# Kernel optimization log

Hardware: AMD Instinct MI355X
Metric: run time of the kernel (lower is better)

Reference implementation:

```python
import jax, jax.numpy as jnp
import numpy as np

HQ, HK, DH = 32, 8, 64
ROPE_BASE = 10000.0


def _rope_tables(T, dtype):
    pos = jnp.arange(T, dtype=jnp.float32)
    inv_freq = 1.0 / (ROPE_BASE ** (jnp.arange(0, DH, 2, dtype=jnp.float32) / DH))
    freqs = pos[:, None] * inv_freq[None, :]          # (T, DH/2)
    cos = jnp.concatenate([jnp.cos(freqs), jnp.cos(freqs)], -1).astype(dtype)  # (T, DH)
    sin = jnp.concatenate([jnp.sin(freqs), jnp.sin(freqs)], -1).astype(dtype)
    return cos, sin


def _rotate_half(t):
    return jnp.concatenate([-t[..., DH // 2:], t[..., :DH // 2]], -1)


def setup_inputs() -> dict:
    key = jax.random.key(0)
    k1, k2, k3, k4 = jax.random.split(key, 4)
    B, T, D = 2, 2048, 2048
    std = 0.02 / np.sqrt(24)
    kv_std = std / np.sqrt(HQ / HK)
    return {
        "x": jax.random.normal(k1, (B, T, D), jnp.float32),
        "Wq": jax.random.normal(k2, (D, HQ * DH), jnp.float32) * std,
        "Wkv": jax.random.normal(k3, (D, 2 * HK * DH), jnp.float32) * kv_std,
        "Wo": jax.random.normal(k4, (HQ * DH, D), jnp.float32) * std,
    }


def reference(x, Wq, Wkv, Wo):
    B, T, D = x.shape
    g = HQ // HK
    scale = DH ** -0.5
    # projections
    q = (x @ Wq).reshape(B, T, HQ, DH).transpose(0, 2, 1, 3)       # (B,Hq,T,Dh)
    kv = (x @ Wkv).reshape(B, T, 2, HK, DH)
    k = kv[:, :, 0].transpose(0, 2, 1, 3)                           # (B,Hk,T,Dh)
    v = kv[:, :, 1].transpose(0, 2, 1, 3)
    # GQA expand: each kv head repeated g times consecutively
    k = jnp.repeat(k, g, axis=1)                                    # (B,Hq,T,Dh)
    v = jnp.repeat(v, g, axis=1)
    # RoPE on q and repeated k
    cos, sin = _rope_tables(T, x.dtype)
    q = q * cos + _rotate_half(q) * sin
    k = k * cos + _rotate_half(k) * sin
    # attention
    scores = jnp.einsum('bhqd,bhkd->bhqk', q, k) * scale            # (B,Hq,T,T)
    causal = jnp.triu(jnp.ones((T, T), bool), 1)
    scores = jnp.where(causal, -jnp.inf, scores)
    attn = jax.nn.softmax(scores.astype(jnp.float32), axis=-1).astype(x.dtype)
    out = jnp.einsum('bhqk,bhkd->bhqd', attn, v)                    # (B,Hq,T,Dh)
    out = out.transpose(0, 2, 1, 3).reshape(B, T, HQ * DH)
    return out @ Wo
```

## Files before the change

kernel.cpp:

```cpp
#include <hip/hip_runtime.h>
#include <hip/hip_bf16.h>

#define DEVI __device__ __forceinline__

typedef __attribute__((ext_vector_type(4))) float f32x4;
typedef __attribute__((ext_vector_type(16))) float f32x16;
typedef __attribute__((ext_vector_type(8))) short s16x8;
typedef __attribute__((ext_vector_type(4))) short s16x4;
typedef __attribute__((ext_vector_type(2))) unsigned u32x2;

DEVI ushort f2bf(float f) {
  union { float f; unsigned u; } v; v.f = f;
  unsigned r = v.u + 0x7FFFu + ((v.u >> 16) & 1u);
  return (ushort)(r >> 16);
}

DEVI void gload_lds16(const void* g, void* l) {
  __builtin_amdgcn_global_load_lds((const __attribute__((address_space(1))) void*)g,
                                   (__attribute__((address_space(3))) void*)l, 16, 0, 0);
}

#define MFMA16 __builtin_amdgcn_mfma_f32_16x16x32_bf16
#define SBAR() __builtin_amdgcn_s_barrier()
#define LGKM0() asm volatile("s_waitcnt lgkmcnt(0)")

DEVI float plswap_max(float x) {
  union { float f; unsigned u; } a; a.f = x;
  u32x2 r = __builtin_amdgcn_permlane32_swap(a.u, a.u, false, false);
  union { unsigned u; float f; } o0, o1; o0.u = r[0]; o1.u = r[1];
  return fmaxf(o0.f, o1.f);
}
DEVI float plswap_sum(float x) {
  union { float f; unsigned u; } a; a.f = x;
  u32x2 r = __builtin_amdgcn_permlane32_swap(a.u, a.u, false, false);
  union { unsigned u; float f; } o0, o1; o0.u = r[0]; o1.u = r[1];
  return o0.f + o1.f;
}

DEVI void stage128q(const ushort* __restrict__ gsrc, int K, ushort* ld, int tid) {
  #pragma unroll
  for (int j = 0; j < 4; ++j) {
    const int ci = j * 256 + tid;
    const int row = ci >> 3, c = ci & 7;
    gload_lds16(gsrc + (size_t)row * K + ((c ^ (row & 7)) << 3),
                ld + (size_t)(j * 256 + (tid & ~63)) * 8);
  }
}
DEVI s16x8 ldfrag(const ushort* tile, int row, int kc) {
  return *(const s16x8*)((const char*)tile + row * 128 + ((kc ^ (row & 7)) << 4));
}

DEVI void stageA32(const ushort* __restrict__ gsrc, int K, ushort* ld, int tid) {
  #pragma unroll
  for (int j = 0; j < 4; ++j) {
    const int ci = j * 256 + tid;
    const int row = ci >> 2, c = ci & 3;
    gload_lds16(gsrc + (size_t)row * K + ((c ^ ((row >> 1) & 3)) << 3),
                ld + (size_t)(j * 256 + (tid & ~63)) * 8);
  }
}
DEVI void stageB32(const ushort* __restrict__ gsrc, int K, ushort* ld, int tid) {
  #pragma unroll
  for (int j = 0; j < 2; ++j) {
    const int ci = j * 256 + tid;
    const int row = ci >> 2, c = ci & 3;
    gload_lds16(gsrc + (size_t)row * K + ((c ^ ((row >> 1) & 3)) << 3),
                ld + (size_t)(j * 256 + (tid & ~63)) * 8);
  }
}
DEVI s16x8 ldfrag32(const ushort* tile, int row, int g) {
  return *(const s16x8*)((const char*)tile + row * 64 + ((g ^ ((row >> 1) & 3)) << 4));
}

DEVI void kloop3(const ushort* __restrict__ A, const ushort* __restrict__ BT,
                 ushort* Asm, ushort* Bsm, int m0, int n0, int K, int NKT,
                 f32x4 (&acc)[4][4], int tid, int wm, int wn, int g, int l15) {
  stage128q(A + (size_t)m0 * K, K, Asm, tid);
  stage128q(BT + (size_t)n0 * K, K, Bsm, tid);
  stage128q(BT + (size_t)n0 * K + 64, K, Bsm + 8192, tid);
  asm volatile("s_waitcnt vmcnt(4)");
  SBAR();

  int rd = 0;
  #pragma unroll 1
  for (int t = 0; t < NKT; ++t) {
    const ushort* Ah = Asm + (t & 1) * 8192;
    const ushort* Bh = Bsm + rd * 8192;
    s16x8 af[4][2], bfr[4][2];

    #pragma unroll
    for (int ks = 0; ks < 2; ++ks) {
      #pragma unroll
      for (int ni = 0; ni < 4; ++ni)
        bfr[ni][ks] = ldfrag(Bh, wn * 64 + ni * 16 + l15, ks * 4 + g);
      #pragma unroll
      for (int mi = 0; mi < 4; ++mi)
        af[mi][ks] = ldfrag(Ah, wm * 64 + mi * 16 + l15, ks * 4 + g);
    }
    if (t + 1 < NKT)
      stage128q(A + (size_t)m0 * K + (t + 1) * 64, K, Asm + ((t + 1) & 1) * 8192, tid);
    int wr = rd + 2; if (wr >= 3) wr -= 3;
    if (t + 2 < NKT)
      stage128q(BT + (size_t)n0 * K + (t + 2) * 64, K, Bsm + wr * 8192, tid);

    LGKM0();
    __builtin_amdgcn_sched_barrier(0);
    __builtin_amdgcn_s_setprio(1);
    #pragma unroll
    for (int mi = 0; mi < 4; ++mi)
      #pragma unroll
      for (int ni = 0; ni < 2; ++ni)
        #pragma unroll
        for (int ks = 0; ks < 2; ++ks)
          acc[mi][ni] = MFMA16(af[mi][ks], bfr[ni][ks], acc[mi][ni], 0, 0, 0);
    #pragma unroll
    for (int mi = 0; mi < 4; ++mi)
      #pragma unroll
      for (int ni = 0; ni < 2; ++ni)
        #pragma unroll
        for (int ks = 0; ks < 2; ++ks)
          acc[mi][2 + ni] = MFMA16(af[mi][ks], bfr[2 + ni][ks], acc[mi][2 + ni], 0, 0, 0);
    __builtin_amdgcn_s_setprio(0);

    if (t + 2 < NKT)      asm volatile("s_waitcnt vmcnt(4)");
    else if (t + 1 < NKT) asm volatile("s_waitcnt vmcnt(0)");
    SBAR();
    rd = (rd == 2) ? 0 : rd + 1;
  }
}

__global__ __launch_bounds__(256) void cast_bf16_k(const float* __restrict__ in,
                                                   ushort* __restrict__ out, int n) {
  int i = (blockIdx.x * 256 + threadIdx.x) * 4;
  if (i >= n) return;
  float4 v = *(const float4*)(in + i);
  ushort4 o;
  o.x = f2bf(v.x); o.y = f2bf(v.y); o.z = f2bf(v.z); o.w = f2bf(v.w);
  *(ushort4*)(out + i) = o;
}

__global__ __launch_bounds__(256) void transpose_cast_k(const float* __restrict__ in,
                                                        ushort* __restrict__ out, int R, int C) {
  __shared__ ushort tile[64][66];
  const int r0 = blockIdx.y * 64, c0 = blockIdx.x * 64;
  const int tid = threadIdx.x;
  #pragma unroll
  for (int j = 0; j < 16; ++j) {
    int idx = j * 256 + tid;
    int r = idx >> 6, c = idx & 63;
    tile[c][r] = f2bf(in[(size_t)(r0 + r) * C + c0 + c]);
  }
  __syncthreads();
  #pragma unroll
  for (int j = 0; j < 16; ++j) {
    int idx = j * 256 + tid;
    int c = idx >> 6, r = idx & 63;
    out[(size_t)(c0 + c) * R + r0 + r] = tile[c][r];
  }
}

__global__ __launch_bounds__(256) void rope_table_k(float2* __restrict__ tab) {
  int idx = blockIdx.x * 256 + threadIdx.x;
  int t = idx >> 5, i = idx & 31;
  float inv = expf(-(float)i * 0.28782313662425575f);
  float ang = (float)t * inv;
  tab[idx] = make_float2(cosf(ang), sinf(ang));
}

__global__ __launch_bounds__(256) void gemm_qkv_3b(const ushort* __restrict__ A,
                                                   const ushort* __restrict__ BT,
                                                   const float2* __restrict__ tab,
                                                   ushort* __restrict__ Qp,
                                                   ushort* __restrict__ Kp,
                                                   ushort* __restrict__ Vp) {
  constexpr int K = 2048, NKT = 32;
  __shared__ __attribute__((aligned(128))) ushort smem[40960];
  ushort* Asm = smem;
  ushort* Bsm = smem + 16384;
  ushort* Ot = smem;

  const int tid = threadIdx.x;
  const int ln = tid & 63, wv = tid >> 6;
  const int g = ln >> 4, l15 = ln & 15, l31 = ln & 31, hi = ln >> 5;
  const int wm = wv >> 1, wn = wv & 1;
  const int m0 = blockIdx.y * 128, n0 = blockIdx.x * 128;

  f32x4 acc[4][4];
  #pragma unroll
  for (int i = 0; i < 4; ++i)
    #pragma unroll
    for (int j = 0; j < 4; ++j) acc[i][j] = (f32x4){0.f, 0.f, 0.f, 0.f};

  kloop3(A, BT, Asm, Bsm, m0, n0, K, NKT, acc, tid, wm, wn, g, l15);

  __syncthreads();
  const int bq = m0 >> 11;
  const int tg0 = m0 & 2047;
  const int type = (n0 < 2048) ? 0 : (n0 < 2560 ? 1 : 2);

  #pragma unroll
  for (int mi = 0; mi < 4; ++mi)
    #pragma unroll
    for (int r = 0; r < 4; ++r) {
      const int tl = wm * 64 + mi * 16 + g * 4 + r;
      const int t = tg0 + tl;
      #pragma unroll
      for (int ni = 0; ni < 4; ++ni) {
        const int cl = wn * 64 + ni * 16 + l15;
        float val = acc[mi][ni][r];
        float outv;
        if (type < 2) {
          float pairv = acc[mi][ni ^ 2][r];
          float2 cs = tab[t * 32 + (ni & 1) * 16 + l15];
          outv = (ni & 2) ? (val * cs.x + pairv * cs.y) : (val * cs.x - pairv * cs.y);
          if (type == 0) outv *= 0.18033688011112042f;
        } else {
          outv = val;
        }
        Ot[tl * 132 + cl] = f2bf(outv);
      }
    }
  __syncthreads();

  #pragma unroll
  for (int it = 0; it < 8; ++it) {
    const int id = wv * 8 + it;
    const int hl = id >> 4, q4 = (id >> 2) & 3, fi = id & 3;
    const int tile = (tg0 >> 5) + q4;
    if (type < 2) {
      const ushort* srow = Ot + (q4 * 32 + l31) * 132 + hl * 64 + fi * 16 + hi * 8;
      union { s16x4 h[2]; s16x8 v; } u;
      u.h[0] = *(const s16x4*)srow;
      u.h[1] = *(const s16x4*)(srow + 4);
      ushort* dst;
      if (type == 0) {
        const int h = (n0 >> 6) + hl;
        dst = Qp + (((size_t)(bq * 32 + h) * 64 + tile) * 4 + fi) * 512 + ln * 8;
      } else {
        const int h = ((n0 - 2048) >> 6) + hl;
        dst = Kp + (((size_t)(bq * 8 + h) * 64 + tile) * 4 + fi) * 512 + ln * 8;
      }
      *(s16x8*)dst = u.v;
    } else {
      const int hk = ((n0 - 2560) >> 6) + hl;
      const int col = hl * 64 + (fi & 1) * 32 + l31;
      const int row0 = q4 * 32 + (fi >> 1) * 16 + hi * 8;
      ushort o[8];
      #pragma unroll
      for (int j = 0; j < 8; ++j) o[j] = Ot[(row0 + j) * 132 + col];
      ushort* dst = Vp + (((size_t)(bq * 8 + hk) * 64 + tile) * 4 + fi) * 512 + ln * 8;
      *(s16x8*)dst = *(const s16x8*)o;
    }
  }
}

__global__ __attribute__((amdgpu_flat_work_group_size(256, 256)))
__attribute__((amdgpu_waves_per_eu(2, 2)))
void gemm_wo_256(const ushort* __restrict__ A,
                 const ushort* __restrict__ BT,
                 float* __restrict__ C) {
  constexpr int N = 2048, K = 2048, NKT = 64, GX = 16, NWG = 256;
  __shared__ __attribute__((aligned(128))) ushort smem[28672];
  ushort* Asm = smem;
  ushort* Bsm = smem + 16384;

  const int tid = threadIdx.x;
  const int ln = tid & 63, wv = tid >> 6;
  const int g = ln >> 4, l15 = ln & 15;
  const int wm = wv >> 1, wn = wv & 1;

  const int orig = blockIdx.x;
  const int wg = (orig & 7) * (NWG / 8) + (orig >> 3);
  const int bx = wg % GX, by = wg / GX;
  const int m0 = by * 256, n0 = bx * 128;

  f32x4 acc[8][4];
  #pragma unroll
  for (int i = 0; i < 8; ++i)
    #pragma unroll
    for (int j = 0; j < 4; ++j) acc[i][j] = (f32x4){0.f, 0.f, 0.f, 0.f};

  stageA32(A + (size_t)m0 * K, K, Asm, tid);
  stageB32(BT + (size_t)n0 * K, K, Bsm, tid);
  stageB32(BT + (size_t)n0 * K + 32, K, Bsm + 4096, tid);
  asm volatile("s_waitcnt vmcnt(2)");
  SBAR();

  int rd = 0;
  #pragma unroll 1
  for (int t = 0; t < NKT; ++t) {
    const ushort* Ah = Asm + (t & 1) * 8192;
    const ushort* Bh = Bsm + rd * 4096;
    s16x8 af[8], bfr[4];

    #pragma unroll
    for (int ni = 0; ni < 4; ++ni)
      bfr[ni] = ldfrag32(Bh, wn * 64 + ni * 16 + l15, g);
    #pragma unroll
    for (int mi = 0; mi < 8; ++mi)
      af[mi] = ldfrag32(Ah, wm * 128 + mi * 16 + l15, g);

    if (t + 1 < NKT)
      stageA32(A + (size_t)m0 * K + (t + 1) * 32, K, Asm + ((t + 1) & 1) * 8192, tid);
    int wr = rd + 2; if (wr >= 3) wr -= 3;
    if (t + 2 < NKT)
      stageB32(BT + (size_t)n0 * K + (t + 2) * 32, K, Bsm + wr * 4096, tid);

    LGKM0();
    __builtin_amdgcn_sched_barrier(0);
    __builtin_amdgcn_s_setprio(1);
    #pragma unroll
    for (int mi = 0; mi < 8; ++mi)
      #pragma unroll
      for (int ni = 0; ni < 4; ++ni)
        acc[mi][ni] = MFMA16(af[mi], bfr[ni], acc[mi][ni], 0, 0, 0);
    __builtin_amdgcn_s_setprio(0);

    if (t + 2 < NKT)      asm volatile("s_waitcnt vmcnt(2)");
    else if (t + 1 < NKT) asm volatile("s_waitcnt vmcnt(0)");
    SBAR();
    rd = (rd == 2) ? 0 : rd + 1;
  }

  #pragma unroll
  for (int mi = 0; mi < 8; ++mi)
    #pragma unroll
    for (int r = 0; r < 4; ++r) {
      int row = m0 + wm * 128 + mi * 16 + g * 4 + r;
      float* crow = C + (size_t)row * N + n0 + wn * 64 + l15;
      #pragma unroll
      for (int ni = 0; ni < 4; ++ni) crow[ni * 16] = acc[mi][ni][r];
    }
}

__global__ __launch_bounds__(256) void attn_k(const ushort* __restrict__ Qp,
                                              const ushort* __restrict__ Kp,
                                              const ushort* __restrict__ Vp,
                                              ushort* __restrict__ O) {
  __shared__ ushort ep[4][32 * 64];
  const int tid = threadIdx.x, wv = tid >> 6, ln = tid & 63;
  const int l31 = ln & 31, hi = ln >> 5;

  const int f = blockIdx.x + gridDim.x * (blockIdx.y + 32 * blockIdx.z);
  const int xcd = f & 7, j = f >> 3;
  const int pr = xcd + 8 * (j & 1);
  const int b = pr >> 3, hk = pr & 7;
  const int s = j >> 1;
  const int hq = hk * 4 + (s & 3);
  const int qtile = 63 - ((s >> 2) * 4 + wv);
  const int qw = qtile * 32;
  const int nt = qtile + 1;

  const ushort* Qh    = Qp + ((size_t)(b * 32 + hq)) * (64 * 2048);
  const ushort* Kbase = Kp + ((size_t)(b * 8 + hk)) * (64 * 2048);
  const ushort* Vbase = Vp + ((size_t)(b * 8 + hk)) * (64 * 2048);
  ushort* lds = ep[wv];

  s16x8 qf[4];
  {
    const ushort* qp_ = Qh + (size_t)qtile * 2048 + ln * 8;
    #pragma unroll
    for (int ks = 0; ks < 4; ++ks) qf[ks] = *(const s16x8*)(qp_ + ks * 512);
  }

  f32x16 z16;
  #pragma unroll
  for (int r = 0; r < 16; ++r) z16[r] = 0.f;

  f32x16 oacc[2];
  #pragma unroll
  for (int dt = 0; dt < 2; ++dt)
    #pragma unroll
    for (int r = 0; r < 16; ++r) oacc[dt][r] = 0.f;
  float m = -1e30f, l = 0.f;

  const ushort* kp = Kbase + ln * 8;
  const ushort* vp = Vbase + ln * 8;

  s16x8 kf[4];
  #pragma unroll
  for (int ks = 0; ks < 4; ++ks) kf[ks] = *(const s16x8*)(kp + ks * 512);
  kp += 2048;

  s16x8 vc[4];
  union pfu { unsigned u[4]; s16x8 v; };
  pfu pf0, pf1;

  #pragma unroll 1
  for (int kt = 0; kt < nt; ++kt) {
    if (kt) {
      __builtin_amdgcn_s_setprio(1);
      oacc[0] = __builtin_amdgcn_mfma_f32_32x32x16_bf16(vc[0], pf0.v, oacc[0], 0, 0, 0);
      oacc[1] = __builtin_amdgcn_mfma_f32_32x32x16_bf16(vc[1], pf0.v, oacc[1], 0, 0, 0);
      oacc[0] = __builtin_amdgcn_mfma_f32_32x32x16_bf16(vc[2], pf1.v, oacc[0], 0, 0, 0);
      oacc[1] = __builtin_amdgcn_mfma_f32_32x32x16_bf16(vc[3], pf1.v, oacc[1], 0, 0, 0);
      __builtin_amdgcn_s_setprio(0);
    }
    #pragma unroll
    for (int fi2 = 0; fi2 < 4; ++fi2) vc[fi2] = *(const s16x8*)(vp + fi2 * 512);
    vp += 2048;

    __builtin_amdgcn_s_setprio(1);
    f32x16 sp = __builtin_amdgcn_mfma_f32_32x32x16_bf16(kf[0], qf[0], z16, 0, 0, 0);
    sp = __builtin_amdgcn_mfma_f32_32x32x16_bf16(kf[1], qf[1], sp, 0, 0, 0);
    sp = __builtin_amdgcn_mfma_f32_32x32x16_bf16(kf[2], qf[2], sp, 0, 0, 0);
    sp = __builtin_amdgcn_mfma_f32_32x32x16_bf16(kf[3], qf[3], sp, 0, 0, 0);
    __builtin_amdgcn_s_setprio(0);

    if (kt + 1 < nt) {
      #pragma unroll
      for (int ks = 0; ks < 4; ++ks) kf[ks] = *(const s16x8*)(kp + ks * 512);
      kp += 2048;
    }

    if (kt == qtile) {
      #pragma unroll
      for (int r = 0; r < 16; ++r) {
        int key = (r & 3) + 8 * (r >> 2) + 4 * hi;
        if (key > l31) sp[r] = -1e30f;
      }
    }

    float t0 = fmaxf(fmaxf(sp[0], sp[1]), sp[2]);
    float t1 = fmaxf(fmaxf(sp[3], sp[4]), sp[5]);
    float t2 = fmaxf(fmaxf(sp[6], sp[7]), sp[8]);
    float t3 = fmaxf(fmaxf(sp[9], sp[10]), sp[11]);
    float t4 = fmaxf(fmaxf(sp[12], sp[13]), sp[14]);
    float u0 = fmaxf(fmaxf(t0, t1), t2);
    float u1 = fmaxf(fmaxf(t3, t4), sp[15]);
    float pm = plswap_max(fmaxf(u0, u1));

    if (__any(pm - m > 8.0f)) {
      float mn = fmaxf(m, pm);
      float alpha = __builtin_amdgcn_exp2f(m - mn);
      m = mn;
      l *= alpha;
      #pragma unroll
      for (int dt = 0; dt < 2; ++dt)
        #pragma unroll
        for (int r = 0; r < 16; ++r) oacc[dt][r] *= alpha;
    }

    #pragma unroll
    for (int r = 0; r < 16; ++r) sp[r] = __builtin_amdgcn_exp2f(sp[r] - m);
    {
      float a0 = sp[0] + sp[1], a1 = sp[2] + sp[3], a2 = sp[4] + sp[5], a3 = sp[6] + sp[7];
      float a4 = sp[8] + sp[9], a5 = sp[10] + sp[11], a6 = sp[12] + sp[13], a7 = sp[14] + sp[15];
      float b0 = a0 + a1, b1 = a2 + a3, b2 = a4 + a5, b3 = a6 + a7;
      l += plswap_sum((b0 + b1) + (b2 + b3));
    }

    unsigned cw[8];
    #pragma unroll
    for (int jj = 0; jj < 8; ++jj) {
      union { __hip_bfloat162 h; unsigned u; } pk;
      pk.h = __float22bfloat162_rn(make_float2(sp[2 * jj], sp[2 * jj + 1]));
      cw[jj] = pk.u;
    }
    {
      u32x2 r;
      r = __builtin_amdgcn_permlane32_swap(cw[0], cw[2], false, false);
      pf0.u[0] = r[0]; pf0.u[2] = r[1];
      r = __builtin_amdgcn_permlane32_swap(cw[1], cw[3], false, false);
      pf0.u[1] = r[0]; pf0.u[3] = r[1];
      r = __builtin_amdgcn_permlane32_swap(cw[4], cw[6], false, false);
      pf1.u[0] = r[0]; pf1.u[2] = r[1];
      r = __builtin_amdgcn_permlane32_swap(cw[5], cw[7], false, false);
      pf1.u[1] = r[0]; pf1.u[3] = r[1];
    }
  }

  __builtin_amdgcn_s_setprio(1);
  oacc[0] = __builtin_amdgcn_mfma_f32_32x32x16_bf16(vc[0], pf0.v, oacc[0], 0, 0, 0);
  oacc[1] = __builtin_amdgcn_mfma_f32_32x32x16_bf16(vc[1], pf0.v, oacc[1], 0, 0, 0);
  oacc[0] = __builtin_amdgcn_mfma_f32_32x32x16_bf16(vc[2], pf1.v, oacc[0], 0, 0, 0);
  oacc[1] = __builtin_amdgcn_mfma_f32_32x32x16_bf16(vc[3], pf1.v, oacc[1], 0, 0, 0);
  __builtin_amdgcn_s_setprio(0);

  float invl = 1.0f / l;
  #pragma unroll
  for (int dt = 0; dt < 2; ++dt)
    #pragma unroll
    for (int r = 0; r < 16; ++r) {
      int d = dt * 32 + (r & 3) + 8 * (r >> 2) + 4 * hi;
      int byte = (l31 * 128 + d * 2) ^ ((l31 & 7) << 4);
      *(ushort*)((char*)lds + byte) = f2bf(oacc[dt][r] * invl);
    }
  const int qr = ln >> 1, half = ln & 1;
  #pragma unroll
  for (int jj = 0; jj < 4; ++jj) {
    int byte = (qr * 128 + half * 64 + jj * 16) ^ ((qr & 7) << 4);
    s16x8 vrow = *(const s16x8*)((const char*)lds + byte);
    *(s16x8*)(O + ((size_t)(b * 2048 + qw + qr)) * 2048 + hq * 64 + half * 32 + jj * 8) = vrow;
  }
}

extern "C" void kernel_launch(void* const* d_in, const int* in_sizes, int n_in,
                              void* d_out, int out_size, void* d_ws, size_t ws_size,
                              hipStream_t stream) {
  const float* x   = (const float*)d_in[0];
  const float* Wq  = (const float*)d_in[1];
  const float* Wkv = (const float*)d_in[2];
  const float* Wo  = (const float*)d_in[3];
  float* out = (float*)d_out;

  char* ws = (char*)d_ws;
  ushort* xb     = (ushort*)(ws);
  ushort* WqkvT  = (ushort*)(ws + 16777216);
  ushort* WoT    = (ushort*)(ws + 29360128);
  float2* tab    = (float2*)(ws + 37748736);
  ushort* Qp     = (ushort*)(ws + 38273024);
  ushort* Kp     = (ushort*)(ws + 55050240);
  ushort* Vp     = (ushort*)(ws + 59244544);
  ushort* Ob     = (ushort*)(ws + 63438848);

  cast_bf16_k<<<8192, 256, 0, stream>>>(x, xb, 2 * 2048 * 2048);
  transpose_cast_k<<<dim3(32, 32), 256, 0, stream>>>(Wq, WqkvT, 2048, 2048);
  transpose_cast_k<<<dim3(16, 32), 256, 0, stream>>>(Wkv, WqkvT + 2048 * 2048, 2048, 1024);
  transpose_cast_k<<<dim3(32, 32), 256, 0, stream>>>(Wo, WoT, 2048, 2048);
  rope_table_k<<<256, 256, 0, stream>>>(tab);
  gemm_qkv_3b<<<dim3(24, 32), 256, 0, stream>>>(xb, WqkvT, tab, Qp, Kp, Vp);
  attn_k<<<dim3(16, 32, 2), 256, 0, stream>>>(Qp, Kp, Vp, Ob);
  gemm_wo_256<<<256, 256, 0, stream>>>(Ob, WoT, out);
}
```

Baseline: 221.3 us.

## Enlarge QKV GEMM tile to 256x128 and revert Wo GEMM to 128x128 tiles

The QKV projection GEMM now uses a 256x128 block tile with a K-step of 64, a bigger LDS buffer, one wave per EU, and an XCD-aware block remap. The RoPE/scale epilogue and head-tiled stores are widened to cover 256 rows. The goal is more operand reuse per block and fewer blocks for the QKV GEMM. The Wo projection goes back to a generic 128x128 kernel built on the shared kloop3 with K-step 64, so that GEMM loses its 256-row tile and swizzled schedule. This trades Wo efficiency for consistency.

```diff
diff --git a/kernel.cpp b/kernel.cpp
--- a/kernel.cpp
+++ b/kernel.cpp
@@ -46,30 +46,17 @@
                 ld + (size_t)(j * 256 + (tid & ~63)) * 8);
   }
 }
+DEVI void stage256q(const ushort* __restrict__ gsrc, int K, ushort* ld, int tid) {
+  #pragma unroll
+  for (int j = 0; j < 8; ++j) {
+    const int ci = j * 256 + tid;
+    const int row = ci >> 3, c = ci & 7;
+    gload_lds16(gsrc + (size_t)row * K + ((c ^ (row & 7)) << 3),
+                ld + (size_t)(j * 256 + (tid & ~63)) * 8);
+  }
+}
 DEVI s16x8 ldfrag(const ushort* tile, int row, int kc) {
   return *(const s16x8*)((const char*)tile + row * 128 + ((kc ^ (row & 7)) << 4));
-}
-
-DEVI void stageA32(const ushort* __restrict__ gsrc, int K, ushort* ld, int tid) {
-  #pragma unroll
-  for (int j = 0; j < 4; ++j) {
-    const int ci = j * 256 + tid;
-    const int row = ci >> 2, c = ci & 3;
-    gload_lds16(gsrc + (size_t)row * K + ((c ^ ((row >> 1) & 3)) << 3),
-                ld + (size_t)(j * 256 + (tid & ~63)) * 8);
-  }
-}
-DEVI void stageB32(const ushort* __restrict__ gsrc, int K, ushort* ld, int tid) {
-  #pragma unroll
-  for (int j = 0; j < 2; ++j) {
-    const int ci = j * 256 + tid;
-    const int row = ci >> 2, c = ci & 3;
-    gload_lds16(gsrc + (size_t)row * K + ((c ^ ((row >> 1) & 3)) << 3),
-                ld + (size_t)(j * 256 + (tid & ~63)) * 8);
-  }
-}
-DEVI s16x8 ldfrag32(const ushort* tile, int row, int g) {
-  return *(const s16x8*)((const char*)tile + row * 64 + ((g ^ ((row >> 1) & 3)) << 4));
 }
 
 DEVI void kloop3(const ushort* __restrict__ A, const ushort* __restrict__ BT,
@@ -167,43 +154,92 @@
   tab[idx] = make_float2(cosf(ang), sinf(ang));
 }
 
-__global__ __launch_bounds__(256) void gemm_qkv_3b(const ushort* __restrict__ A,
-                                                   const ushort* __restrict__ BT,
-                                                   const float2* __restrict__ tab,
-                                                   ushort* __restrict__ Qp,
-                                                   ushort* __restrict__ Kp,
-                                                   ushort* __restrict__ Vp) {
-  constexpr int K = 2048, NKT = 32;
-  __shared__ __attribute__((aligned(128))) ushort smem[40960];
+__global__ __attribute__((amdgpu_flat_work_group_size(256, 256)))
+__attribute__((amdgpu_waves_per_eu(1, 1)))
+void gemm_qkv_fat(const ushort* __restrict__ A,
+                  const ushort* __restrict__ BT,
+                  const float2* __restrict__ tab,
+                  ushort* __restrict__ Qp,
+                  ushort* __restrict__ Kp,
+                  ushort* __restrict__ Vp) {
+  constexpr int K = 2048, NKT = 32, GX = 24, NWG = 384;
+  __shared__ __attribute__((aligned(128))) ushort smem[57344];
   ushort* Asm = smem;
-  ushort* Bsm = smem + 16384;
+  ushort* Bsm = smem + 32768;
   ushort* Ot = smem;
 
   const int tid = threadIdx.x;
   const int ln = tid & 63, wv = tid >> 6;
   const int g = ln >> 4, l15 = ln & 15, l31 = ln & 31, hi = ln >> 5;
   const int wm = wv >> 1, wn = wv & 1;
-  const int m0 = blockIdx.y * 128, n0 = blockIdx.x * 128;
-
-  f32x4 acc[4][4];
-  #pragma unroll
-  for (int i = 0; i < 4; ++i)
+
+  const int orig = blockIdx.x;
+  const int wg = (orig & 7) * (NWG / 8) + (orig >> 3);
+  const int bx = wg % GX, by = wg / GX;
+  const int m0 = by * 256, n0 = bx * 128;
+
+  f32x4 acc[8][4];
+  #pragma unroll
+  for (int i = 0; i < 8; ++i)
     #pragma unroll
     for (int j = 0; j < 4; ++j) acc[i][j] = (f32x4){0.f, 0.f, 0.f, 0.f};
 
-  kloop3(A, BT, Asm, Bsm, m0, n0, K, NKT, acc, tid, wm, wn, g, l15);
+  stage256q(A + (size_t)m0 * K, K, Asm, tid);
+  stage128q(BT + (size_t)n0 * K, K, Bsm, tid);
+  stage128q(BT + (size_t)n0 * K + 64, K, Bsm + 8192, tid);
+  asm volatile("s_waitcnt vmcnt(4)");
+  SBAR();
+
+  int rd = 0;
+  #pragma unroll 1
+  for (int t = 0; t < NKT; ++t) {
+    const ushort* Ah = Asm + (t & 1) * 16384;
+    const ushort* Bh = Bsm + rd * 8192;
+
+    if (t + 1 < NKT)
+      stage256q(A + (size_t)m0 * K + (t + 1) * 64, K, Asm + ((t + 1) & 1) * 16384, tid);
+    int wr = rd + 2; if (wr >= 3) wr -= 3;
+    if (t + 2 < NKT)
+      stage128q(BT + (size_t)n0 * K + (t + 2) * 64, K, Bsm + wr * 8192, tid);
+
+    #pragma unroll
+    for (int ks = 0; ks < 2; ++ks) {
+      s16x8 af[8], bfr[4];
+      #pragma unroll
+      for (int ni = 0; ni < 4; ++ni)
+        bfr[ni] = ldfrag(Bh, wn * 64 + ni * 16 + l15, ks * 4 + g);
+      #pragma unroll
+      for (int mi = 0; mi < 8; ++mi)
+        af[mi] = ldfrag(Ah, wm * 128 + mi * 16 + l15, ks * 4 + g);
+      LGKM0();
+      __builtin_amdgcn_sched_barrier(0);
+      __builtin_amdgcn_s_setprio(1);
+      #pragma unroll
+      for (int mi = 0; mi < 8; ++mi)
+        #pragma unroll
+        for (int ni = 0; ni < 4; ++ni)
+          acc[mi][ni] = MFMA16(af[mi], bfr[ni], acc[mi][ni], 0, 0, 0);
+      __builtin_amdgcn_s_setprio(0);
+    }
+
+    if (t + 2 < NKT)      asm volatile("s_waitcnt vmcnt(4)");
+    else if (t + 1 < NKT) asm volatile("s_waitcnt vmcnt(0)");
+    SBAR();
+    rd = (rd == 2) ? 0 : rd + 1;
+  }
 
   __syncthreads();
-  const int bq = m0 >> 11;
-  const int tg0 = m0 & 2047;
-  const int type = (n0 < 2048) ? 0 : (n0 < 2560 ? 1 : 2);
-
-  #pragma unroll
-  for (int mi = 0; mi < 4; ++mi)
+  const int bq = by >> 3;
+  const int tb0 = (by & 7) * 256;
+  const int type = (bx < 16) ? 0 : (bx < 20 ? 1 : 2);
+  constexpr int OST = 132;
+
+  #pragma unroll
+  for (int mi = 0; mi < 8; ++mi)
     #pragma unroll
     for (int r = 0; r < 4; ++r) {
-      const int tl = wm * 64 + mi * 16 + g * 4 + r;
-      const int t = tg0 + tl;
+      const int tl = wm * 128 + mi * 16 + g * 4 + r;
+      const int t = tb0 + tl;
       #pragma unroll
       for (int ni = 0; ni < 4; ++ni) {
         const int cl = wn * 64 + ni * 16 + l15;
@@ -217,50 +253,47 @@
         } else {
           outv = val;
         }
-        Ot[tl * 132 + cl] = f2bf(outv);
+        Ot[tl * OST + cl] = f2bf(outv);
       }
     }
   __syncthreads();
 
   #pragma unroll
-  for (int it = 0; it < 8; ++it) {
-    const int id = wv * 8 + it;
-    const int hl = id >> 4, q4 = (id >> 2) & 3, fi = id & 3;
-    const int tile = (tg0 >> 5) + q4;
+  for (int it = 0; it < 16; ++it) {
+    const int id = wv * 16 + it;
+    const int hl = id >> 5, q8 = (id >> 2) & 7, fi = id & 3;
+    const int tile = (by & 7) * 8 + q8;
     if (type < 2) {
-      const ushort* srow = Ot + (q4 * 32 + l31) * 132 + hl * 64 + fi * 16 + hi * 8;
+      const ushort* srow = Ot + (q8 * 32 + l31) * OST + hl * 64 + fi * 16 + hi * 8;
       union { s16x4 h[2]; s16x8 v; } u;
       u.h[0] = *(const s16x4*)srow;
       u.h[1] = *(const s16x4*)(srow + 4);
       ushort* dst;
       if (type == 0) {
-        const int h = (n0 >> 6) + hl;
+        const int h = bx * 2 + hl;
         dst = Qp + (((size_t)(bq * 32 + h) * 64 + tile) * 4 + fi) * 512 + ln * 8;
       } else {
-        const int h = ((n0 - 2048) >> 6) + hl;
+        const int h = (bx - 16) * 2 + hl;
         dst = Kp + (((size_t)(bq * 8 + h) * 64 + tile) * 4 + fi) * 512 + ln * 8;
       }
       *(s16x8*)dst = u.v;
     } else {
-      const int hk = ((n0 - 2560) >> 6) + hl;
+      const int hk = (bx - 20) * 2 + hl;
       const int col = hl * 64 + (fi & 1) * 32 + l31;
-      const int row0 = q4 * 32 + (fi >> 1) * 16 + hi * 8;
+      const int row0 = q8 * 32 + (fi >> 1) * 16 + hi * 8;
       ushort o[8];
       #pragma unroll
-      for (int j = 0; j < 8; ++j) o[j] = Ot[(row0 + j) * 132 + col];
+      for (int j2 = 0; j2 < 8; ++j2) o[j2] = Ot[(row0 + j2) * OST + col];
       ushort* dst = Vp + (((size_t)(bq * 8 + hk) * 64 + tile) * 4 + fi) * 512 + ln * 8;
       *(s16x8*)dst = *(const s16x8*)o;
     }
   }
 }
 
-__global__ __attribute__((amdgpu_flat_work_group_size(256, 256)))
-__attribute__((amdgpu_waves_per_eu(2, 2)))
-void gemm_wo_256(const ushort* __restrict__ A,
-                 const ushort* __restrict__ BT,
-                 float* __restrict__ C) {
-  constexpr int N = 2048, K = 2048, NKT = 64, GX = 16, NWG = 256;
-  __shared__ __attribute__((aligned(128))) ushort smem[28672];
+__global__ __launch_bounds__(256) void gemm_bt_3b(const ushort* __restrict__ A,
+                                                  const ushort* __restrict__ BT,
+                                                  float* __restrict__ C, int M, int N, int K) {
+  __shared__ __attribute__((aligned(128))) ushort smem[40960];
   ushort* Asm = smem;
   ushort* Bsm = smem + 16384;
 
@@ -268,65 +301,22 @@
   const int ln = tid & 63, wv = tid >> 6;
   const int g = ln >> 4, l15 = ln & 15;
   const int wm = wv >> 1, wn = wv & 1;
-
-  const int orig = blockIdx.x;
-  const int wg = (orig & 7) * (NWG / 8) + (orig >> 3);
-  const int bx = wg % GX, by = wg / GX;
-  const int m0 = by * 256, n0 = bx * 128;
-
-  f32x4 acc[8][4];
-  #pragma unroll
-  for (int i = 0; i < 8; ++i)
+  const int m0 = blockIdx.y * 128, n0 = blockIdx.x * 128;
+  const int NKT = K / 64;
+
+  f32x4 acc[4][4];
+  #pragma unroll
+  for (int i = 0; i < 4; ++i)
     #pragma unroll
     for (int j = 0; j < 4; ++j) acc[i][j] = (f32x4){0.f, 0.f, 0.f, 0.f};
 
-  stageA32(A + (size_t)m0 * K, K, Asm, tid);
-  stageB32(BT + (size_t)n0 * K, K, Bsm, tid);
-  stageB32(BT + (size_t)n0 * K + 32, K, Bsm + 4096, tid);
-  asm volatile("s_waitcnt vmcnt(2)");
-  SBAR();
-
-  int rd = 0;
-  #pragma unroll 1
-  for (int t = 0; t < NKT; ++t) {
-    const ushort* Ah = Asm + (t & 1) * 8192;
-    const ushort* Bh = Bsm + rd * 4096;
-    s16x8 af[8], bfr[4];
-
-    #pragma unroll
-    for (int ni = 0; ni < 4; ++ni)
-      bfr[ni] = ldfrag32(Bh, wn * 64 + ni * 16 + l15, g);
-    #pragma unroll
-    for (int mi = 0; mi < 8; ++mi)
-      af[mi] = ldfrag32(Ah, wm * 128 + mi * 16 + l15, g);
-
-    if (t + 1 < NKT)
-      stageA32(A + (size_t)m0 * K + (t + 1) * 32, K, Asm + ((t + 1) & 1) * 8192, tid);
-    int wr = rd + 2; if (wr >= 3) wr -= 3;
-    if (t + 2 < NKT)
-      stageB32(BT + (size_t)n0 * K + (t + 2) * 32, K, Bsm + wr * 4096, tid);
-
-    LGKM0();
-    __builtin_amdgcn_sched_barrier(0);
-    __builtin_amdgcn_s_setprio(1);
-    #pragma unroll
-    for (int mi = 0; mi < 8; ++mi)
-      #pragma unroll
-      for (int ni = 0; ni < 4; ++ni)
-        acc[mi][ni] = MFMA16(af[mi], bfr[ni], acc[mi][ni], 0, 0, 0);
-    __builtin_amdgcn_s_setprio(0);
-
-    if (t + 2 < NKT)      asm volatile("s_waitcnt vmcnt(2)");
-    else if (t + 1 < NKT) asm volatile("s_waitcnt vmcnt(0)");
-    SBAR();
-    rd = (rd == 2) ? 0 : rd + 1;
-  }
-
-  #pragma unroll
-  for (int mi = 0; mi < 8; ++mi)
+  kloop3(A, BT, Asm, Bsm, m0, n0, K, NKT, acc, tid, wm, wn, g, l15);
+
+  #pragma unroll
+  for (int mi = 0; mi < 4; ++mi)
     #pragma unroll
     for (int r = 0; r < 4; ++r) {
-      int row = m0 + wm * 128 + mi * 16 + g * 4 + r;
+      int row = m0 + wm * 64 + mi * 16 + g * 4 + r;
       float* crow = C + (size_t)row * N + n0 + wn * 64 + l15;
       #pragma unroll
       for (int ni = 0; ni < 4; ++ni) crow[ni * 16] = acc[mi][ni][r];
@@ -519,7 +509,7 @@
   transpose_cast_k<<<dim3(16, 32), 256, 0, stream>>>(Wkv, WqkvT + 2048 * 2048, 2048, 1024);
   transpose_cast_k<<<dim3(32, 32), 256, 0, stream>>>(Wo, WoT, 2048, 2048);
   rope_table_k<<<256, 256, 0, stream>>>(tab);
-  gemm_qkv_3b<<<dim3(24, 32), 256, 0, stream>>>(xb, WqkvT, tab, Qp, Kp, Vp);
+  gemm_qkv_fat<<<384, 256, 0, stream>>>(xb, WqkvT, tab, Qp, Kp, Vp);
   attn_k<<<dim3(16, 32, 2), 256, 0, stream>>>(Qp, Kp, Vp, Ob);
-  gemm_wo_256<<<256, 256, 0, stream>>>(Ob, WoT, out);
-}
+  gemm_bt_3b<<<dim3(16, 32), 256, 0, stream>>>(Ob, WoT, out, 4096, 2048, 2048);
+}
```

Result: slower. 236.5 us (+6.9%).
